# Performance work log

Measured on AMD Instinct MI355X. Metric: run time of the kernel, lower is better.

Reference implementation:

```python
import jax, jax.numpy as jnp
import numpy as np

N, E, H, D, F_IN = 50000, 400000, 2, 128, 5
EPS = 1e-5  # BatchNorm eps

def _bn(x, gamma, beta, rm, rv):
    # eval-mode BatchNorm1d using running stats
    return (x - rm) * jax.lax.rsqrt(rv + EPS) * gamma + beta

def setup_inputs() -> dict:
    key = jax.random.key(0)
    ks = jax.random.split(key, 24)
    r = lambda i, shape, s=1.0: jax.random.normal(ks[i], shape, jnp.float32) * s
    u = lambda i, shape: jax.random.uniform(ks[i], shape, jnp.float32)
    return {
        "h": r(0, (N, F_IN)),
        "edge_index": jax.random.randint(ks[1], (2, E), 0, N),
        "edge_weight": r(2, (E, 1)),
        # BatchNorm1d(5)
        "gamma1": 1.0 + r(3, (F_IN,), 0.1), "beta1": r(4, (F_IN,), 0.1),
        "rm1": r(5, (F_IN,), 0.1), "rv1": 0.5 + u(6, (F_IN,)),
        # GATv2Conv params (lin_l, lin_r with bias; lin_edge no bias; att; out bias)
        "Wl": r(7, (F_IN, H * D), 0.2), "bl": r(8, (H * D,), 0.1),
        "Wr": r(9, (F_IN, H * D), 0.2), "br": r(10, (H * D,), 0.1),
        "We": r(11, (1, H * D), 0.2),
        "att": r(12, (H, D), 0.2),
        "bias_gat": r(13, (D,), 0.1),
        # fc1 + BatchNorm1d(128)
        "W1": r(14, (D, D), 0.08), "b1": r(15, (D,), 0.1),
        "gamma2": 1.0 + r(16, (D,), 0.1), "beta2": r(17, (D,), 0.1),
        "rm2": r(18, (D,), 0.1), "rv2": 0.5 + u(19, (D,)),
        # fc2
        "W2": r(20, (D, F_IN), 0.08), "b2": r(21, (F_IN,), 0.1),
    }

def reference(h, edge_index, edge_weight, gamma1, beta1, rm1, rv1,
              Wl, bl, Wr, br, We, att, bias_gat,
              W1, b1, gamma2, beta2, rm2, rv2, W2, b2):
    src, dst = edge_index[0], edge_index[1]
    h = _bn(h, gamma1, beta1, rm1, rv1)
    xl = (h @ Wl + bl).reshape(N, H, D)   # source transform (messages)
    xr = (h @ Wr + br).reshape(N, H, D)   # destination transform
    e = (edge_weight @ We).reshape(E, H, D)
    # GATv2: score = att . leaky_relu(x_j + x_i + edge_emb), slope 0.2
    z = jax.nn.leaky_relu(xl[src] + xr[dst] + e, 0.2)          # [E,H,D]
    logits = jnp.einsum('ehd,hd->eh', z, att)                   # [E,H]
    # segment softmax over edges sharing a destination node
    mx = jax.ops.segment_max(logits, dst, num_segments=N)       # [N,H]
    ex = jnp.exp(logits - mx[dst])
    den = jax.ops.segment_sum(ex, dst, num_segments=N)
    alpha = ex / (den[dst] + 1e-16)                             # [E,H]
    msg = xl[src] * alpha[:, :, None]                           # [E,H,D]
    ssum = jax.ops.segment_sum(msg, dst, num_segments=N)        # [N,H,D]
    cnt = jax.ops.segment_sum(jnp.ones((E,), jnp.float32), dst, num_segments=N)
    out = ssum / jnp.maximum(cnt, 1.0)[:, None, None]           # aggr='mean'
    out = out.mean(axis=1) + bias_gat                           # concat=False -> head mean
    out = out @ W1 + b1
    out = _bn(out, gamma2, beta2, rm2, rv2)
    out = jax.nn.leaky_relu(out, 0.01)
    # dropout is identity in eval mode
    out = out @ W2 + b2                                         # [N,5]
    return out
```

## Files before the change

### kernel.cpp

```cpp
#include <hip/hip_runtime.h>

#define N_NODES 50000
#define N_EDGES 400000
#define F_INP 5
#define HD 256
#define BN_EPS 1e-5f

typedef short v8s __attribute__((ext_vector_type(8)));
typedef float v4f __attribute__((ext_vector_type(4)));
typedef unsigned v4u __attribute__((ext_vector_type(4)));

#define OFF_HBN 0
#define OFF_ACC 400000
#define OFF_BPK 1200000

__device__ __forceinline__ unsigned short f2bf(float f) {
    unsigned u = __float_as_uint(f);
    return (unsigned short)((u + 0x7FFFu + ((u >> 16) & 1u)) >> 16);
}
__device__ __forceinline__ unsigned pk2(float a, float b) {
    return (unsigned)f2bf(a) | ((unsigned)f2bf(b) << 16);
}

__device__ __forceinline__ float wcat(int k, int c, const float* Wl, const float* Wr,
                                      const float* We, const float* bl, const float* br) {
    if (k < 5)   return Wl[k * HD + c];
    if (k < 10)  return Wr[(k - 5) * HD + c];
    if (k == 10) return We[c];
    return bl[c] + br[c];
}

__global__ void k_prep(const float* __restrict__ h, const float* __restrict__ g1,
                       const float* __restrict__ be1, const float* __restrict__ rm1,
                       const float* __restrict__ rv1,
                       const float* __restrict__ Wl, const float* __restrict__ bl,
                       const float* __restrict__ Wr, const float* __restrict__ br,
                       const float* __restrict__ We, const float* __restrict__ att,
                       float* __restrict__ hbn8, float* __restrict__ acc,
                       unsigned* __restrict__ Bpk) {
    int i = blockIdx.x * blockDim.x + threadIdx.x;
    if (i < N_NODES * 16) acc[i] = 0.f;
    if (i < N_NODES * 8) {
        int f = i & 7, n = i >> 3;
        float v = 0.f;
        if (f < F_INP) {
            float x = h[n * F_INP + f];
            v = (x - rm1[f]) * rsqrtf(rv1[f] + BN_EPS) * g1[f] + be1[f];
        }
        hbn8[i] = v;
    }
    if (i < 1024) {
        int t = i >> 6, l = i & 63;
        int g = l >> 4, c = t * 16 + (l & 15);
        unsigned d0 = 0, d1 = 0;
        if (g < 3) {
            int kb = 4 * g;
            d0 = pk2(wcat(kb + 0, c, Wl, Wr, We, bl, br),
                     wcat(kb + 1, c, Wl, Wr, We, bl, br));
            d1 = pk2(wcat(kb + 2, c, Wl, Wr, We, bl, br),
                     wcat(kb + 3, c, Wl, Wr, We, bl, br));
        }
        Bpk[(t * 64 + l) * 2 + 0] = d0;
        Bpk[(t * 64 + l) * 2 + 1] = d1;
    }
}

__launch_bounds__(256)
__global__ void k_edge(const float* __restrict__ hbn8, const int* __restrict__ ei,
                       const float* __restrict__ ew, const unsigned* __restrict__ Bpk,
                       const float* __restrict__ att, float* __restrict__ acc) {
    int lane = threadIdx.x & 63;
    int wv = threadIdx.x >> 6;
    int g = lane >> 4, e16 = lane & 15;

    v8s B[16];
    float AT[16];
#pragma unroll
    for (int t = 0; t < 16; ++t) {
        unsigned d0 = Bpk[(t * 64 + lane) * 2 + 0];
        unsigned d1 = Bpk[(t * 64 + lane) * 2 + 1];
        v4u u = {d0, d1, 0u, 0u};
        B[t] = __builtin_bit_cast(v8s, u);
        AT[t] = att[t * 16 + e16];
    }

    int wid = blockIdx.x * 4 + wv;
    int nw = gridDim.x * 4;
    const int NT = N_EDGES / 16;

    int q13 = lane / 13;
    int j13 = lane - q13 * 13;
    bool sc_act = lane < 52;
    int kk = (j13 < 6) ? j13 - 1 : j13 - 7;
    int kc = min(max(kk, 0), 4);

    float x0 = 0, x1 = 0, x2 = 0, x3 = 0, x4 = 0,
          x5 = 0, x6 = 0, x7 = 0, x8 = 0, x9 = 0, x10 = 0;
    int dst_reg = 0;
    if (wid < NT && lane < 16) {
        int e = wid * 16 + lane;
        int src = ei[e];
        dst_reg = ei[N_EDGES + e];
        x10 = ew[e];
        float4 s4 = *(const float4*)&hbn8[src * 8];
        x0 = s4.x; x1 = s4.y; x2 = s4.z; x3 = s4.w;
        x4 = hbn8[src * 8 + 4];
        float4 d4 = *(const float4*)&hbn8[dst_reg * 8];
        x5 = d4.x; x6 = d4.y; x7 = d4.z; x8 = d4.w;
        x9 = hbn8[dst_reg * 8 + 4];
    }

    for (int tile = wid; tile < NT; tile += nw) {
        float b0 = __shfl(x0, e16), b1 = __shfl(x1, e16), b2 = __shfl(x2, e16),
              b3 = __shfl(x3, e16), b4 = __shfl(x4, e16), b5 = __shfl(x5, e16),
              b6 = __shfl(x6, e16), b7 = __shfl(x7, e16), b8 = __shfl(x8, e16),
              b9 = __shfl(x9, e16), b10 = __shfl(x10, e16);
        int dst_b = __shfl(dst_reg, e16);

        float a0 = (g == 0) ? b0 : (g == 1) ? b4 : b8;
        float a1 = (g == 0) ? b1 : (g == 1) ? b5 : b9;
        float a2 = (g == 0) ? b2 : (g == 1) ? b6 : b10;
        float a3 = (g == 0) ? b3 : (g == 1) ? b7 : 1.0f;
        unsigned ua0 = (g < 3) ? pk2(a0, a1) : 0u;
        unsigned ua1 = (g < 3) ? pk2(a2, a3) : 0u;
        v4u uav = {ua0, ua1, 0u, 0u};
        v8s A = __builtin_bit_cast(v8s, uav);

        int tn = tile + nw;
        if (tn < NT && lane < 16) {
            int e = tn * 16 + lane;
            int src = ei[e];
            dst_reg = ei[N_EDGES + e];
            x10 = ew[e];
            float4 s4 = *(const float4*)&hbn8[src * 8];
            x0 = s4.x; x1 = s4.y; x2 = s4.z; x3 = s4.w;
            x4 = hbn8[src * 8 + 4];
            float4 d4 = *(const float4*)&hbn8[dst_reg * 8];
            x5 = d4.x; x6 = d4.y; x7 = d4.z; x8 = d4.w;
            x9 = hbn8[dst_reg * 8 + 4];
        }

        float p00 = 0.f, p01 = 0.f, p02 = 0.f, p03 = 0.f;
        float p10 = 0.f, p11 = 0.f, p12 = 0.f, p13v = 0.f;
        v4f zero = {0.f, 0.f, 0.f, 0.f};
#pragma unroll
        for (int t = 0; t < 8; ++t) {
            v4f c = __builtin_amdgcn_mfma_f32_16x16x32_bf16(A, B[t], zero, 0, 0, 0);
            p00 += AT[t] * fmaf(0.66666667f, fabsf(c[0]), c[0]);
            p01 += AT[t] * fmaf(0.66666667f, fabsf(c[1]), c[1]);
            p02 += AT[t] * fmaf(0.66666667f, fabsf(c[2]), c[2]);
            p03 += AT[t] * fmaf(0.66666667f, fabsf(c[3]), c[3]);
        }
#pragma unroll
        for (int t = 8; t < 16; ++t) {
            v4f c = __builtin_amdgcn_mfma_f32_16x16x32_bf16(A, B[t], zero, 0, 0, 0);
            p10 += AT[t] * fmaf(0.66666667f, fabsf(c[0]), c[0]);
            p11 += AT[t] * fmaf(0.66666667f, fabsf(c[1]), c[1]);
            p12 += AT[t] * fmaf(0.66666667f, fabsf(c[2]), c[2]);
            p13v += AT[t] * fmaf(0.66666667f, fabsf(c[3]), c[3]);
        }
#pragma unroll
        for (int m = 1; m <= 8; m <<= 1) {
            p00 += __shfl_xor(p00, m); p01 += __shfl_xor(p01, m);
            p02 += __shfl_xor(p02, m); p03 += __shfl_xor(p03, m);
            p10 += __shfl_xor(p10, m); p11 += __shfl_xor(p11, m);
            p12 += __shfl_xor(p12, m); p13v += __shfl_xor(p13v, m);
        }
        float e00 = __expf(0.6f * p00), e01 = __expf(0.6f * p01);
        float e02 = __expf(0.6f * p02), e03 = __expf(0.6f * p03);
        float e10 = __expf(0.6f * p10), e11 = __expf(0.6f * p11);
        float e12 = __expf(0.6f * p12), e13 = __expf(0.6f * p13v);
        float tA0 = (lane & 1) ? e01 : e00;
        float tA1 = (lane & 1) ? e03 : e02;
        float exA = (lane & 2) ? tA1 : tA0;
        float tB0 = (lane & 1) ? e11 : e10;
        float tB1 = (lane & 1) ? e13 : e12;
        float exB = (lane & 2) ? tB1 : tB0;

        if (sc_act) {
#pragma unroll
            for (int it = 0; it < 4; ++it) {
                int es = it * 4 + q13;
                float h0 = __shfl(b0, es), h1 = __shfl(b1, es), h2 = __shfl(b2, es),
                      h3 = __shfl(b3, es), h4 = __shfl(b4, es);
                int de = __shfl(dst_b, es);
                float xh0 = __shfl(exA, it * 16 + q13);
                float xh1 = __shfl(exB, it * 16 + q13);
                float hsel = h0;
                hsel = (kc == 1) ? h1 : hsel;
                hsel = (kc == 2) ? h2 : hsel;
                hsel = (kc == 3) ? h3 : hsel;
                hsel = (kc == 4) ? h4 : hsel;
                float base = (j13 < 6) ? xh0 : xh1;
                float v = base * hsel;
                v = (j13 == 0) ? xh0 : v;
                v = (j13 == 6) ? xh1 : v;
                v = (j13 == 12) ? 1.0f : v;
                atomicAdd(&acc[de * 16 + j13], v);
            }
        }
    }
}

__launch_bounds__(256, 1)
__global__ void k_mlp(const float* __restrict__ acc,
                      const float* __restrict__ Wl, const float* __restrict__ bl,
                      const float* __restrict__ bias_gat,
                      const float* __restrict__ W1, const float* __restrict__ b1,
                      const float* __restrict__ g2, const float* __restrict__ be2,
                      const float* __restrict__ rm2, const float* __restrict__ rv2,
                      const float* __restrict__ W2, const float* __restrict__ b2,
                      float* __restrict__ out) {
    __shared__ float wsh[128 * 128];
    __shared__ float xsh[8][128];
    __shared__ float wlsh[5 * 256 + 256 + 128];
    __shared__ float accsh[8][16];
    int t = threadIdx.x;
    for (int i = t; i < 128 * 128 / 4; i += 256)
        ((float4*)wsh)[i] = ((const float4*)W1)[i];
    for (int i = t; i < 5 * 256; i += 256) wlsh[i] = Wl[i];
    wlsh[1280 + t] = bl[t];
    if (t < 128) wlsh[1536 + t] = bias_gat[t];
    __syncthreads();
    const float* WL = wlsh;
    const float* BL = wlsh + 1280;
    const float* BG = wlsh + 1536;

    int nl = t >> 5;
    int jg = t & 31;
    int j4 = jg * 4;

    const int ngroups = (N_NODES + 7) / 8;
    for (int gr = blockIdx.x; gr < ngroups; gr += gridDim.x) {
        int n = gr * 8 + nl;
        if (t < 128) {
            int node = gr * 8 + (t >> 4);
            accsh[t >> 4][t & 15] = (node < N_NODES) ? acc[node * 16 + (t & 15)] : 0.f;
        }
        __syncthreads();
        bool valid = n < N_NODES;
        if (valid) {
            float den0 = accsh[nl][0], den1 = accsh[nl][6], cntv = accsh[nl][12];
            float r0 = 1.f / (den0 + 1e-16f), r1 = 1.f / (den1 + 1e-16f);
            float scale = 0.5f / fmaxf(cntv, 1.f);
            float c0 = den0 * r0 * scale, c1 = den1 * r1 * scale;
            float T0[F_INP], T1[F_INP];
#pragma unroll
            for (int f = 0; f < F_INP; ++f) {
                T0[f] = accsh[nl][1 + f] * r0 * scale;
                T1[f] = accsh[nl][7 + f] * r1 * scale;
            }
#pragma unroll
            for (int q = 0; q < 4; ++q) {
                int d = j4 + q;
                float xv = c0 * BL[d] + c1 * BL[128 + d];
#pragma unroll
                for (int f = 0; f < F_INP; ++f)
                    xv += T0[f] * WL[f * HD + d] + T1[f] * WL[f * HD + 128 + d];
                xsh[nl][d] = xv + BG[d];
            }
            float4 a4 = *(const float4*)&b1[j4];
#pragma unroll 8
            for (int k = 0; k < 128; ++k) {
                float xv = xsh[nl][k];
                float4 w = *(const float4*)&wsh[k * 128 + j4];
                a4.x += xv * w.x; a4.y += xv * w.y;
                a4.z += xv * w.z; a4.w += xv * w.w;
            }
            float4 rm = *(const float4*)&rm2[j4];
            float4 rv = *(const float4*)&rv2[j4];
            float4 gg = *(const float4*)&g2[j4];
            float4 bb = *(const float4*)&be2[j4];
            float a[4];
            a[0] = (a4.x - rm.x) * rsqrtf(rv.x + BN_EPS) * gg.x + bb.x;
            a[1] = (a4.y - rm.y) * rsqrtf(rv.y + BN_EPS) * gg.y + bb.y;
            a[2] = (a4.z - rm.z) * rsqrtf(rv.z + BN_EPS) * gg.z + bb.z;
            a[3] = (a4.w - rm.w) * rsqrtf(rv.w + BN_EPS) * gg.w + bb.w;
#pragma unroll
            for (int q = 0; q < 4; ++q) a[q] = fmaxf(a[q], 0.01f * a[q]);
            float pf[5] = {0.f, 0.f, 0.f, 0.f, 0.f};
#pragma unroll
            for (int q = 0; q < 4; ++q)
#pragma unroll
                for (int f = 0; f < 5; ++f) pf[f] += a[q] * W2[(j4 + q) * 5 + f];
#pragma unroll
            for (int m = 16; m; m >>= 1)
#pragma unroll
                for (int f = 0; f < 5; ++f) pf[f] += __shfl_xor(pf[f], m);
            if (jg == 0) {
#pragma unroll
                for (int f = 0; f < 5; ++f) out[n * 5 + f] = pf[f] + b2[f];
            }
        }
        __syncthreads();
    }
}

extern "C" void kernel_launch(void* const* d_in, const int* in_sizes, int n_in,
                              void* d_out, int out_size, void* d_ws, size_t ws_size,
                              hipStream_t stream) {
    const float* h    = (const float*)d_in[0];
    const int*   ei   = (const int*)d_in[1];
    const float* ew   = (const float*)d_in[2];
    const float* g1   = (const float*)d_in[3];
    const float* be1  = (const float*)d_in[4];
    const float* rm1  = (const float*)d_in[5];
    const float* rv1  = (const float*)d_in[6];
    const float* Wl   = (const float*)d_in[7];
    const float* bl   = (const float*)d_in[8];
    const float* Wr   = (const float*)d_in[9];
    const float* br   = (const float*)d_in[10];
    const float* We   = (const float*)d_in[11];
    const float* att  = (const float*)d_in[12];
    const float* bias_gat = (const float*)d_in[13];
    const float* W1   = (const float*)d_in[14];
    const float* b1   = (const float*)d_in[15];
    const float* g2   = (const float*)d_in[16];
    const float* be2  = (const float*)d_in[17];
    const float* rm2  = (const float*)d_in[18];
    const float* rv2  = (const float*)d_in[19];
    const float* W2   = (const float*)d_in[20];
    const float* b2   = (const float*)d_in[21];

    float* ws  = (float*)d_ws;
    float* hbn = ws + OFF_HBN;
    float* acc = ws + OFF_ACC;
    unsigned* Bpk = (unsigned*)(ws + OFF_BPK);

    k_prep<<<(N_NODES * 16 + 255) / 256, 256, 0, stream>>>(
        h, g1, be1, rm1, rv1, Wl, bl, Wr, br, We, att, hbn, acc, Bpk);
    k_edge<<<1024, 256, 0, stream>>>(hbn, ei, ew, Bpk, att, acc);
    k_mlp<<<512, 256, 0, stream>>>(acc, Wl, bl, bias_gat, W1, b1, g2, be2, rm2, rv2, W2, b2,
                                   (float*)d_out);
}
```

Baseline: 100.4 us.

## Fold Wl projection and fc1 into a packed 12x128 weight, one node per thread

Precomputes, on the device, the product of the lin_l weights and biases (plus the GAT bias) with W1, and folds the BatchNorm into a scale and shift. This shrinks the per-node MLP from a 128x128 matvec to 12 inputs per hidden unit. k_mlp is rewritten so each thread handles one node and reads the packed weights as uniform loads, dropping the large shared-memory staging and block syncs. The cost is an extra single-block packing kernel, serial over 13x128 dot products, added to the launch chain.

```diff
diff --git a/kernel.cpp b/kernel.cpp
--- a/kernel.cpp
+++ b/kernel.cpp
@@ -10,9 +10,11 @@
 typedef float v4f __attribute__((ext_vector_type(4)));
 typedef unsigned v4u __attribute__((ext_vector_type(4)));
 
-#define OFF_HBN 0
-#define OFF_ACC 400000
-#define OFF_BPK 1200000
+#define OFF_HBN  0
+#define OFF_ACC  400000
+#define OFF_BPK  1200000
+#define OFF_WF   1202048
+#define OFF_W2P  1204096
 
 __device__ __forceinline__ unsigned short f2bf(float f) {
     unsigned u = __float_as_uint(f);
@@ -63,6 +65,36 @@
         Bpk[(t * 64 + l) * 2 + 0] = d0;
         Bpk[(t * 64 + l) * 2 + 1] = d1;
     }
+}
+
+__global__ void k_pack2(const float* __restrict__ Wl, const float* __restrict__ bl,
+                        const float* __restrict__ bias_gat,
+                        const float* __restrict__ W1, const float* __restrict__ b1,
+                        const float* __restrict__ g2, const float* __restrict__ be2,
+                        const float* __restrict__ rm2, const float* __restrict__ rv2,
+                        const float* __restrict__ W2,
+                        float* __restrict__ Wf, float* __restrict__ W2p) {
+    int c = blockIdx.x * blockDim.x + threadIdx.x;
+    if (c >= 128) return;
+#pragma unroll
+    for (int k = 0; k < 13; ++k) {
+        const float* base = (k == 0) ? bl
+                          : (k == 1) ? bl + 128
+                          : (k < 7)  ? Wl + (k - 2) * HD
+                          : (k < 12) ? Wl + (k - 7) * HD + 128
+                                     : bias_gat;
+        float sum = 0.f;
+        for (int d = 0; d < 128; ++d) sum += base[d] * W1[d * 128 + c];
+        if (k == 12) sum += b1[c];
+        Wf[c * 16 + k] = sum;
+    }
+    float sc = g2[c] * rsqrtf(rv2[c] + BN_EPS);
+    Wf[c * 16 + 13] = sc;
+    Wf[c * 16 + 14] = be2[c] - rm2[c] * sc;
+    Wf[c * 16 + 15] = 0.f;
+#pragma unroll
+    for (int f = 0; f < 8; ++f)
+        W2p[c * 8 + f] = (f < 5) ? W2[c * 5 + f] : 0.f;
 }
 
 __launch_bounds__(256)
@@ -202,98 +234,48 @@
     }
 }
 
-__launch_bounds__(256, 1)
-__global__ void k_mlp(const float* __restrict__ acc,
-                      const float* __restrict__ Wl, const float* __restrict__ bl,
-                      const float* __restrict__ bias_gat,
-                      const float* __restrict__ W1, const float* __restrict__ b1,
-                      const float* __restrict__ g2, const float* __restrict__ be2,
-                      const float* __restrict__ rm2, const float* __restrict__ rv2,
-                      const float* __restrict__ W2, const float* __restrict__ b2,
+__launch_bounds__(256)
+__global__ void k_mlp(const float* __restrict__ acc, const float* __restrict__ Wf,
+                      const float* __restrict__ W2p, const float* __restrict__ b2,
                       float* __restrict__ out) {
-    __shared__ float wsh[128 * 128];
-    __shared__ float xsh[8][128];
-    __shared__ float wlsh[5 * 256 + 256 + 128];
-    __shared__ float accsh[8][16];
-    int t = threadIdx.x;
-    for (int i = t; i < 128 * 128 / 4; i += 256)
-        ((float4*)wsh)[i] = ((const float4*)W1)[i];
-    for (int i = t; i < 5 * 256; i += 256) wlsh[i] = Wl[i];
-    wlsh[1280 + t] = bl[t];
-    if (t < 128) wlsh[1536 + t] = bias_gat[t];
-    __syncthreads();
-    const float* WL = wlsh;
-    const float* BL = wlsh + 1280;
-    const float* BG = wlsh + 1536;
-
-    int nl = t >> 5;
-    int jg = t & 31;
-    int j4 = jg * 4;
-
-    const int ngroups = (N_NODES + 7) / 8;
-    for (int gr = blockIdx.x; gr < ngroups; gr += gridDim.x) {
-        int n = gr * 8 + nl;
-        if (t < 128) {
-            int node = gr * 8 + (t >> 4);
-            accsh[t >> 4][t & 15] = (node < N_NODES) ? acc[node * 16 + (t & 15)] : 0.f;
-        }
-        __syncthreads();
-        bool valid = n < N_NODES;
-        if (valid) {
-            float den0 = accsh[nl][0], den1 = accsh[nl][6], cntv = accsh[nl][12];
-            float r0 = 1.f / (den0 + 1e-16f), r1 = 1.f / (den1 + 1e-16f);
-            float scale = 0.5f / fmaxf(cntv, 1.f);
-            float c0 = den0 * r0 * scale, c1 = den1 * r1 * scale;
-            float T0[F_INP], T1[F_INP];
-#pragma unroll
-            for (int f = 0; f < F_INP; ++f) {
-                T0[f] = accsh[nl][1 + f] * r0 * scale;
-                T1[f] = accsh[nl][7 + f] * r1 * scale;
-            }
-#pragma unroll
-            for (int q = 0; q < 4; ++q) {
-                int d = j4 + q;
-                float xv = c0 * BL[d] + c1 * BL[128 + d];
-#pragma unroll
-                for (int f = 0; f < F_INP; ++f)
-                    xv += T0[f] * WL[f * HD + d] + T1[f] * WL[f * HD + 128 + d];
-                xsh[nl][d] = xv + BG[d];
-            }
-            float4 a4 = *(const float4*)&b1[j4];
-#pragma unroll 8
-            for (int k = 0; k < 128; ++k) {
-                float xv = xsh[nl][k];
-                float4 w = *(const float4*)&wsh[k * 128 + j4];
-                a4.x += xv * w.x; a4.y += xv * w.y;
-                a4.z += xv * w.z; a4.w += xv * w.w;
-            }
-            float4 rm = *(const float4*)&rm2[j4];
-            float4 rv = *(const float4*)&rv2[j4];
-            float4 gg = *(const float4*)&g2[j4];
-            float4 bb = *(const float4*)&be2[j4];
-            float a[4];
-            a[0] = (a4.x - rm.x) * rsqrtf(rv.x + BN_EPS) * gg.x + bb.x;
-            a[1] = (a4.y - rm.y) * rsqrtf(rv.y + BN_EPS) * gg.y + bb.y;
-            a[2] = (a4.z - rm.z) * rsqrtf(rv.z + BN_EPS) * gg.z + bb.z;
-            a[3] = (a4.w - rm.w) * rsqrtf(rv.w + BN_EPS) * gg.w + bb.w;
-#pragma unroll
-            for (int q = 0; q < 4; ++q) a[q] = fmaxf(a[q], 0.01f * a[q]);
-            float pf[5] = {0.f, 0.f, 0.f, 0.f, 0.f};
-#pragma unroll
-            for (int q = 0; q < 4; ++q)
-#pragma unroll
-                for (int f = 0; f < 5; ++f) pf[f] += a[q] * W2[(j4 + q) * 5 + f];
-#pragma unroll
-            for (int m = 16; m; m >>= 1)
-#pragma unroll
-                for (int f = 0; f < 5; ++f) pf[f] += __shfl_xor(pf[f], m);
-            if (jg == 0) {
-#pragma unroll
-                for (int f = 0; f < 5; ++f) out[n * 5 + f] = pf[f] + b2[f];
-            }
-        }
-        __syncthreads();
-    }
+    int n = blockIdx.x * blockDim.x + threadIdx.x;
+    if (n >= N_NODES) return;
+    const float* ar = acc + (size_t)n * 16;
+    float4 A0 = *(const float4*)(ar + 0);
+    float4 A1 = *(const float4*)(ar + 4);
+    float4 A2 = *(const float4*)(ar + 8);
+    float cnt = ar[12];
+    float r0 = 1.f / (A0.x + 1e-16f);
+    float r1 = 1.f / (A1.z + 1e-16f);
+    float scale = 0.5f / fmaxf(cnt, 1.f);
+    float s0 = scale * r0, s1 = scale * r1;
+    float m0 = A0.x * s0, m1 = A1.z * s1;
+    float m2 = A0.y * s0, m3 = A0.z * s0, m4 = A0.w * s0, m5 = A1.x * s0, m6 = A1.y * s0;
+    float m7 = A1.w * s1, m8 = A2.x * s1, m9 = A2.y * s1, m10 = A2.z * s1, m11 = A2.w * s1;
+
+    float o0 = 0.f, o1 = 0.f, o2 = 0.f, o3 = 0.f, o4 = 0.f;
+#pragma unroll 4
+    for (int c = 0; c < 128; ++c) {
+        const float* wr = &Wf[c * 16];
+        float a = wr[12];
+        a += m0 * wr[0] + m1 * wr[1] + m2 * wr[2] + m3 * wr[3];
+        a += m4 * wr[4] + m5 * wr[5] + m6 * wr[6] + m7 * wr[7];
+        a += m8 * wr[8] + m9 * wr[9] + m10 * wr[10] + m11 * wr[11];
+        a = fmaf(a, wr[13], wr[14]);
+        a = fmaxf(a, 0.01f * a);
+        const float* w2 = &W2p[c * 8];
+        o0 = fmaf(a, w2[0], o0);
+        o1 = fmaf(a, w2[1], o1);
+        o2 = fmaf(a, w2[2], o2);
+        o3 = fmaf(a, w2[3], o3);
+        o4 = fmaf(a, w2[4], o4);
+    }
+    float* op = out + (size_t)n * 5;
+    op[0] = o0 + b2[0];
+    op[1] = o1 + b2[1];
+    op[2] = o2 + b2[2];
+    op[3] = o3 + b2[3];
+    op[4] = o4 + b2[4];
 }
 
 extern "C" void kernel_launch(void* const* d_in, const int* in_sizes, int n_in,
@@ -326,10 +308,13 @@
     float* hbn = ws + OFF_HBN;
     float* acc = ws + OFF_ACC;
     unsigned* Bpk = (unsigned*)(ws + OFF_BPK);
+    float* Wf  = ws + OFF_WF;
+    float* W2p = ws + OFF_W2P;
 
     k_prep<<<(N_NODES * 16 + 255) / 256, 256, 0, stream>>>(
         h, g1, be1, rm1, rv1, Wl, bl, Wr, br, We, att, hbn, acc, Bpk);
+    k_pack2<<<1, 128, 0, stream>>>(Wl, bl, bias_gat, W1, b1, g2, be2, rm2, rv2, W2,
+                                   Wf, W2p);
     k_edge<<<1024, 256, 0, stream>>>(hbn, ei, ew, Bpk, att, acc);
-    k_mlp<<<512, 256, 0, stream>>>(acc, Wl, bl, bias_gat, W1, b1, g2, be2, rm2, rv2, W2, b2,
-                                   (float*)d_out);
-}
+    k_mlp<<<(N_NODES + 255) / 256, 256, 0, stream>>>(acc, Wf, W2p, b2, (float*)d_out);
+}
```

Measured after the change: 121.2 us. 1.21x slower.
